# Optimization experiments

Measured on AMD Instinct MI355X. Metric: run time of the kernel, lower is better.

Reference implementation:

```python
import jax, jax.numpy as jnp
import numpy as np

D = 128          # voxel grid resolution per axis
N = 500_000      # number of active voxels
C = 64           # channels (in == out)
K = 27           # 3x3x3 kernel volume
EPS = 1e-5


def _build_geometry():
    """Random active voxel set + submanifold 3x3x3 neighbor index pairs."""
    rng = np.random.default_rng(0)
    lin = rng.choice(D ** 3, size=N, replace=False).astype(np.int64)
    zc, yc, xc = lin // (D * D), (lin // D) % D, lin % D
    order = np.argsort(lin)
    sorted_lin = lin[order]
    nbr = np.zeros((K, N), np.int32)
    valid = np.zeros((K, N), np.float32)
    k = 0
    for dz in (-1, 0, 1):
        for dy in (-1, 0, 1):
            for dx in (-1, 0, 1):
                nz, ny, nx = zc + dz, yc + dy, xc + dx
                inb = (nz >= 0) & (nz < D) & (ny >= 0) & (ny < D) & (nx >= 0) & (nx < D)
                nlin = nz * D * D + ny * D + nx
                pos = np.clip(np.searchsorted(sorted_lin, nlin), 0, N - 1)
                found = inb & (sorted_lin[pos] == nlin)
                nbr[k] = np.where(found, order[pos], 0).astype(np.int32)
                valid[k] = found.astype(np.float32)
                k += 1
    return jnp.asarray(nbr), jnp.asarray(valid)


def setup_inputs() -> dict:
    key = jax.random.key(0)
    k_feat, k_w1, k_w2 = jax.random.split(key, 3)
    nbr_idx, valid = _build_geometry()
    scale = 1.0 / np.sqrt(K * C)  # kaiming-ish fan-in init
    return {
        "features": jax.random.normal(k_feat, (N, C), jnp.float32),
        "nbr_idx": nbr_idx,
        "valid": valid,
        "W1": jax.random.normal(k_w1, (K, C, C), jnp.float32) * scale,
        "gamma1": jnp.ones((C,), jnp.float32),
        "beta1": jnp.zeros((C,), jnp.float32),
        "W2": jax.random.normal(k_w2, (K, C, C), jnp.float32) * scale,
        "gamma2": jnp.ones((C,), jnp.float32),
        "beta2": jnp.zeros((C,), jnp.float32),
    }


def _subm_conv(x, W, nbr_idx, valid):
    """Submanifold 3D conv as gather-GEMM-accumulate over K kernel offsets."""
    def step(acc, kw):
        Wk, nk, vk = kw
        return acc + (x[nk] * vk[:, None]) @ Wk, None  # [N,Cin] @ [Cin,Cout]
    acc0 = jnp.zeros((x.shape[0], W.shape[-1]), x.dtype)
    acc, _ = jax.lax.scan(step, acc0, (W, nbr_idx, valid))
    return acc


def _batchnorm(f, gamma, beta):
    """Training-mode BN over active voxels (biased variance, like torch)."""
    mean = jnp.mean(f, axis=0)
    var = jnp.mean(jnp.square(f - mean), axis=0)
    return (f - mean) * jax.lax.rsqrt(var + EPS) * gamma + beta


def reference(features, nbr_idx, valid, W1, gamma1, beta1, W2, gamma2, beta2):
    out = _subm_conv(features, W1, nbr_idx, valid)
    out = jax.nn.relu(_batchnorm(out, gamma1, beta1))
    out = _subm_conv(out, W2, nbr_idx, valid)
    out = _batchnorm(out, gamma2, beta2)
    return jax.nn.relu(out + features)  # identity shortcut (Cin==Cout, stride=1)
```

## Files before the change

### kernel.cpp

```cpp
#include <hip/hip_runtime.h>
#include <hip/hip_bf16.h>
#include <stdint.h>

typedef __attribute__((ext_vector_type(8))) short short8;
typedef __attribute__((ext_vector_type(4))) float floatx4;

__device__ __forceinline__ float bf2f(unsigned short u) {
    union { unsigned int ui; float f; } v; v.ui = ((unsigned int)u) << 16; return v.f;
}
__device__ __forceinline__ unsigned short f2bf(float f) {
    union { float f; unsigned int u; } v; v.f = f;
    unsigned int u = v.u;
    unsigned int r = (u + 0x7fffu + ((u >> 16) & 1u)) >> 16;
    return (unsigned short)r;
}

__global__ __launch_bounds__(256)
void convert_bf16(const float* __restrict__ in, unsigned short* __restrict__ out, int n4) {
    int i = blockIdx.x * blockDim.x + threadIdx.x;
    int stride = gridDim.x * blockDim.x;
    for (; i < n4; i += stride) {
        float4 v = ((const float4*)in)[i];
        ushort4 o;
        o.x = f2bf(v.x); o.y = f2bf(v.y); o.z = f2bf(v.z); o.w = f2bf(v.w);
        ((ushort4*)out)[i] = o;
    }
}

__global__ __launch_bounds__(256)
void encode_kernel(const int* __restrict__ nbr, const float* __restrict__ valid,
                   int* __restrict__ enc, int nvox, int nvoxp) {
    int k = blockIdx.y;
    int r = blockIdx.x * 256 + threadIdx.x;
    int v = -1;
    if (r < nvox) {
        float f = valid[(size_t)k * nvox + r];
        int ix = nbr[(size_t)k * nvox + r];
        v = (f != 0.f) ? ix : -1;
    }
    enc[(size_t)k * nvoxp + r] = v;
}

__global__ __launch_bounds__(256)
void pack_w(const float* __restrict__ W1, const float* __restrict__ W2,
            unsigned short* __restrict__ Wp1, unsigned short* __restrict__ Wp2) {
    int bi = blockIdx.x;
    const float* W = (bi < 27) ? W1 : W2;
    unsigned short* Wp = (bi < 27) ? Wp1 : Wp2;
    int kk = bi % 27;
    int t = threadIdx.x;
    int lane = t & 63, grp = t >> 6;
    int q = lane >> 4, l15 = lane & 15;
    for (int c8 = grp; c8 < 8; c8 += 4) {
        int ks = c8 >> 2, nt = c8 & 3;
        unsigned short* dst = Wp + (((kk*2 + ks)*4 + nt)*64 + lane)*8;
        const float* src = W + kk*4096 + (ks*32 + q*8)*64 + nt*16 + l15;
        #pragma unroll
        for (int j = 0; j < 8; ++j) dst[j] = f2bf(src[j*64]);
    }
}

__global__ __launch_bounds__(256, 4)
void conv_kernel(const unsigned short* __restrict__ xin, const int* __restrict__ enc,
                 const unsigned short* __restrict__ Wp, const unsigned short* __restrict__ zrow,
                 unsigned short* __restrict__ yout, float* __restrict__ sums,
                 int nvox, int nvoxp) {
    int t = threadIdx.x;
    int wave = t >> 6, lane = t & 63;
    int q = lane >> 4, l15 = lane & 15;
    int m0 = blockIdx.x * 256 + wave * 64;

    floatx4 acc[4][4];
    #pragma unroll
    for (int s = 0; s < 4; ++s)
        #pragma unroll
        for (int nt = 0; nt < 4; ++nt) acc[s][nt] = (floatx4){0.f, 0.f, 0.f, 0.f};

    for (int kk = 0; kk < 27; ++kk) {
        int e_all = enc[(size_t)kk * nvoxp + m0 + lane];
        const unsigned short* rp[4];
        #pragma unroll
        for (int s = 0; s < 4; ++s) {
            int es = __builtin_amdgcn_ds_bpermute((s*16 + l15) * 4, e_all);
            rp[s] = (es >= 0) ? (xin + (size_t)es * 64) : zrow;
        }
        short8 av[2][4];
        #pragma unroll
        for (int ks = 0; ks < 2; ++ks)
            #pragma unroll
            for (int s = 0; s < 4; ++s)
                av[ks][s] = *(const short8*)(rp[s] + ks*32 + q*8);

        #pragma unroll
        for (int ks = 0; ks < 2; ++ks) {
            const unsigned short* wb = Wp + ((kk*2 + ks)*4)*512 + lane*8;
            #pragma unroll
            for (int nt = 0; nt < 4; ++nt) {
                short8 bv = *(const short8*)(wb + nt*512);
                #pragma unroll
                for (int s = 0; s < 4; ++s)
                    acc[s][nt] = __builtin_amdgcn_mfma_f32_16x16x32_bf16(av[ks][s], bv, acc[s][nt], 0, 0, 0);
            }
        }
    }

    #pragma unroll
    for (int s = 0; s < 4; ++s) {
        int rowb = m0 + s*16 + q*4;
        #pragma unroll
        for (int r = 0; r < 4; ++r) {
            if (rowb + r < nvox) {
                unsigned short* yo = yout + (size_t)(rowb + r)*64 + l15;
                #pragma unroll
                for (int nt = 0; nt < 4; ++nt)
                    yo[nt*16] = f2bf(acc[s][nt][r]);
            }
        }
    }

    __shared__ float sred[128];
    if (t < 128) sred[t] = 0.f;
    __syncthreads();
    #pragma unroll
    for (int nt = 0; nt < 4; ++nt) {
        float s_ = 0.f, q_ = 0.f;
        #pragma unroll
        for (int s = 0; s < 4; ++s)
            #pragma unroll
            for (int r = 0; r < 4; ++r) {
                float v = acc[s][nt][r];
                s_ += v; q_ += v*v;
            }
        atomicAdd(&sred[nt*16 + l15], s_);
        atomicAdd(&sred[64 + nt*16 + l15], q_);
    }
    __syncthreads();
    if (t < 128) atomicAdd(&sums[t], sred[t]);
}

__global__ void finalize_kernel(const float* __restrict__ sums, const float* __restrict__ gamma,
                                const float* __restrict__ beta, float* __restrict__ ab, float invn) {
    int c = threadIdx.x;
    if (c < 64) {
        float mean = sums[c] * invn;
        float var  = sums[64 + c] * invn - mean*mean;
        float a = gamma[c] * rsqrtf(var + 1e-5f);
        ab[c] = a;
        ab[64 + c] = beta[c] - mean * a;
    }
}

__global__ __launch_bounds__(256)
void bnrelu_kernel(unsigned short* __restrict__ y, const float* __restrict__ ab, int n4) {
    int i = blockIdx.x * blockDim.x + threadIdx.x;
    int stride = gridDim.x * blockDim.x;
    for (; i < n4; i += stride) {
        uint2 v = ((const uint2*)y)[i];
        int c0 = (i*4) & 63;
        float f0 = fmaxf(ab[c0]   * bf2f((unsigned short)(v.x & 0xffffu)) + ab[64 + c0],   0.f);
        float f1 = fmaxf(ab[c0+1] * bf2f((unsigned short)(v.x >> 16))     + ab[64 + c0+1], 0.f);
        float f2 = fmaxf(ab[c0+2] * bf2f((unsigned short)(v.y & 0xffffu)) + ab[64 + c0+2], 0.f);
        float f3 = fmaxf(ab[c0+3] * bf2f((unsigned short)(v.y >> 16))     + ab[64 + c0+3], 0.f);
        uint2 o;
        o.x = (unsigned int)f2bf(f0) | ((unsigned int)f2bf(f1) << 16);
        o.y = (unsigned int)f2bf(f2) | ((unsigned int)f2bf(f3) << 16);
        ((uint2*)y)[i] = o;
    }
}

__global__ __launch_bounds__(256)
void final_kernel(const unsigned short* __restrict__ y2, const float* __restrict__ feat,
                  const float* __restrict__ ab, float* __restrict__ out, int ntot2) {
    int i = blockIdx.x * blockDim.x + threadIdx.x;
    int stride = gridDim.x * blockDim.x;
    for (; i < ntot2; i += stride) {
        unsigned int v = ((const unsigned int*)y2)[i];
        int c0 = (i*2) & 63;
        float2 f = ((const float2*)feat)[i];
        float r0 = fmaxf(ab[c0]   * bf2f((unsigned short)(v & 0xffffu)) + ab[64 + c0]   + f.x, 0.f);
        float r1 = fmaxf(ab[c0+1] * bf2f((unsigned short)(v >> 16))     + ab[64 + c0+1] + f.y, 0.f);
        ((float2*)out)[i] = make_float2(r0, r1);
    }
}

extern "C" void kernel_launch(void* const* d_in, const int* in_sizes, int n_in,
                              void* d_out, int out_size, void* d_ws, size_t ws_size,
                              hipStream_t stream) {
    const float* features = (const float*)d_in[0];
    const int*   nbr      = (const int*)d_in[1];
    const float* valid    = (const float*)d_in[2];
    const float* W1       = (const float*)d_in[3];
    const float* gamma1   = (const float*)d_in[4];
    const float* beta1    = (const float*)d_in[5];
    const float* W2       = (const float*)d_in[6];
    const float* gamma2   = (const float*)d_in[7];
    const float* beta2    = (const float*)d_in[8];
    float* out = (float*)d_out;

    int nvox  = in_sizes[0] / 64;
    int nvoxp = (nvox + 255) & ~255;
    size_t featB = (size_t)nvox * 64 * 2;

    char* ob = (char*)d_out;
    unsigned short* xb = (unsigned short*)ob;
    unsigned short* y1 = (unsigned short*)(ob + featB);

    char* ws = (char*)d_ws;
    float* stats = (float*)ws;
    float* sums1 = stats;
    float* sums2 = stats + 128;
    float* ab1   = stats + 256;
    float* ab2   = stats + 384;
    const unsigned short* zrow = (const unsigned short*)(ws + 2048);
    unsigned short* Wp1 = (unsigned short*)(ws + 4096);
    unsigned short* Wp2 = (unsigned short*)(ws + 4096 + 221184);
    int* enc = (int*)(ws + 524288);
    size_t encB = (size_t)27 * nvoxp * 4;
    unsigned short* y2 = (unsigned short*)(ws + 524288 + encB);

    hipMemsetAsync(ws, 0, 4096, stream);

    convert_bf16<<<2048, 256, 0, stream>>>(features, xb, nvox * 16);
    pack_w<<<54, 256, 0, stream>>>(W1, W2, Wp1, Wp2);
    dim3 eg(nvoxp / 256, 27);
    encode_kernel<<<eg, 256, 0, stream>>>(nbr, valid, enc, nvox, nvoxp);

    int convGrid = nvoxp / 256;
    conv_kernel<<<convGrid, 256, 0, stream>>>(xb, enc, Wp1, zrow, y1, sums1, nvox, nvoxp);
    finalize_kernel<<<1, 64, 0, stream>>>(sums1, gamma1, beta1, ab1, 1.0f / nvox);
    bnrelu_kernel<<<2048, 256, 0, stream>>>(y1, ab1, nvox * 16);
    conv_kernel<<<convGrid, 256, 0, stream>>>(y1, enc, Wp2, zrow, y2, sums2, nvox, nvoxp);
    finalize_kernel<<<1, 64, 0, stream>>>(sums2, gamma2, beta2, ab2, 1.0f / nvox);
    final_kernel<<<4096, 256, 0, stream>>>(y2, features, ab2, out, nvox * 32);
}
```

Measured before the change: 782.1 us.

## Double-buffer neighbor gathers against MFMA and stage neighbor indices in LDS

Each block now preloads all 27 neighbor-index rows for its 256 voxels into shared memory. The kernel-offset loop becomes a two-stage software pipeline: the gathered feature rows for the next offset are loaded into a second register buffer while MFMAs run on the current one, with sched barriers and raised wave priority around the MFMA phase. The aim is to hide the latency of random global gathers behind matrix math and to drop the per-iteration bpermute. In exchange it uses about 27 KB of LDS per block and twice the A-fragment registers, so the occupancy hint drops from 4 to 3 blocks.

```diff
diff --git a/kernel.cpp b/kernel.cpp
--- a/kernel.cpp
+++ b/kernel.cpp
@@ -60,49 +60,86 @@
     }
 }
 
-__global__ __launch_bounds__(256, 4)
+__global__ __launch_bounds__(256, 3)
 void conv_kernel(const unsigned short* __restrict__ xin, const int* __restrict__ enc,
                  const unsigned short* __restrict__ Wp, const unsigned short* __restrict__ zrow,
                  unsigned short* __restrict__ yout, float* __restrict__ sums,
                  int nvox, int nvoxp) {
+    __shared__ int lds_enc[27 * 256];
+    __shared__ float sred[128];
+
     int t = threadIdx.x;
     int wave = t >> 6, lane = t & 63;
     int q = lane >> 4, l15 = lane & 15;
     int m0 = blockIdx.x * 256 + wave * 64;
 
+    {
+        size_t base = (size_t)blockIdx.x * 256;
+        #pragma unroll
+        for (int kk = 0; kk < 27; ++kk)
+            lds_enc[kk * 256 + t] = enc[(size_t)kk * nvoxp + base + t];
+    }
+    if (t < 128) sred[t] = 0.f;
+    __syncthreads();
+
     floatx4 acc[4][4];
     #pragma unroll
     for (int s = 0; s < 4; ++s)
         #pragma unroll
         for (int nt = 0; nt < 4; ++nt) acc[s][nt] = (floatx4){0.f, 0.f, 0.f, 0.f};
 
-    for (int kk = 0; kk < 27; ++kk) {
-        int e_all = enc[(size_t)kk * nvoxp + m0 + lane];
-        const unsigned short* rp[4];
-        #pragma unroll
-        for (int s = 0; s < 4; ++s) {
-            int es = __builtin_amdgcn_ds_bpermute((s*16 + l15) * 4, e_all);
-            rp[s] = (es >= 0) ? (xin + (size_t)es * 64) : zrow;
-        }
-        short8 av[2][4];
-        #pragma unroll
-        for (int ks = 0; ks < 2; ++ks)
-            #pragma unroll
-            for (int s = 0; s < 4; ++s)
-                av[ks][s] = *(const short8*)(rp[s] + ks*32 + q*8);
-
-        #pragma unroll
-        for (int ks = 0; ks < 2; ++ks) {
-            const unsigned short* wb = Wp + ((kk*2 + ks)*4)*512 + lane*8;
-            #pragma unroll
-            for (int nt = 0; nt < 4; ++nt) {
-                short8 bv = *(const short8*)(wb + nt*512);
-                #pragma unroll
-                for (int s = 0; s < 4; ++s)
-                    acc[s][nt] = __builtin_amdgcn_mfma_f32_16x16x32_bf16(av[ks][s], bv, acc[s][nt], 0, 0, 0);
-            }
-        }
-    }
+    int eb = wave * 64 + l15;
+
+#define LOAD_ES(es, kk) { _Pragma("unroll") \
+    for (int s_ = 0; s_ < 4; ++s_) es[s_] = lds_enc[(kk) * 256 + eb + s_ * 16]; }
+
+#define GATHER(av, es) { _Pragma("unroll") \
+    for (int s_ = 0; s_ < 4; ++s_) { \
+        const unsigned short* rp_ = (es[s_] >= 0) ? (xin + (size_t)es[s_] * 64) : zrow; \
+        av[0][s_] = *(const short8*)(rp_ + q * 8); \
+        av[1][s_] = *(const short8*)(rp_ + 32 + q * 8); \
+    } }
+
+#define MFMA_PHASE(av, kk) { \
+    __builtin_amdgcn_s_setprio(1); \
+    _Pragma("unroll") for (int ks_ = 0; ks_ < 2; ++ks_) { \
+        const unsigned short* wb_ = Wp + (((kk) * 2 + ks_) * 4) * 512 + lane * 8; \
+        _Pragma("unroll") for (int nt_ = 0; nt_ < 4; ++nt_) { \
+            short8 bv_ = *(const short8*)(wb_ + nt_ * 512); \
+            _Pragma("unroll") for (int s_ = 0; s_ < 4; ++s_) \
+                acc[s_][nt_] = __builtin_amdgcn_mfma_f32_16x16x32_bf16(av[ks_][s_], bv_, acc[s_][nt_], 0, 0, 0); \
+        } \
+    } \
+    __builtin_amdgcn_s_setprio(0); \
+}
+
+    short8 avA[2][4], avB[2][4];
+    int esE[4], esO[4];
+
+    LOAD_ES(esE, 0);
+    LOAD_ES(esO, 1);
+    GATHER(avA, esE);
+    LOAD_ES(esE, 2);
+
+    #pragma unroll 1
+    for (int kkp = 0; kkp < 26; kkp += 2) {
+        GATHER(avB, esO);
+        int k3 = kkp + 3; if (k3 > 26) k3 = 26;
+        LOAD_ES(esO, k3);
+        __builtin_amdgcn_sched_barrier(0);
+        MFMA_PHASE(avA, kkp);
+
+        GATHER(avA, esE);
+        int k4 = kkp + 4; if (k4 > 26) k4 = 26;
+        LOAD_ES(esE, k4);
+        __builtin_amdgcn_sched_barrier(0);
+        MFMA_PHASE(avB, kkp + 1);
+    }
+    MFMA_PHASE(avA, 26);
+
+#undef LOAD_ES
+#undef GATHER
+#undef MFMA_PHASE
 
     #pragma unroll
     for (int s = 0; s < 4; ++s) {
@@ -118,9 +155,6 @@
         }
     }
 
-    __shared__ float sred[128];
-    if (t < 128) sred[t] = 0.f;
-    __syncthreads();
     #pragma unroll
     for (int nt = 0; nt < 4; ++nt) {
         float s_ = 0.f, q_ = 0.f;
```

Result: slower. 858.4 us (+9.8%).

## Software-pipeline gather loads in conv kernel with triple-buffered A fragments

Applied to the files above, without the earlier changes.

Restructures the conv kernel so each wave handles 32 rows instead of 64, doubling the grid. The gathers and enc index loads for later kernel offsets are issued two offsets ahead through three rotating register buffers, with sched_barrier and setprio around the MFMA phase. The aim is to hide gather latency behind MFMAs and raise the number of waves in flight. In exchange, each wave reloads the B weights for only 32 rows, so weight traffic per row doubles, and register pressure rises.

```diff
diff --git a/kernel.cpp b/kernel.cpp
--- a/kernel.cpp
+++ b/kernel.cpp
@@ -65,47 +65,83 @@
                  const unsigned short* __restrict__ Wp, const unsigned short* __restrict__ zrow,
                  unsigned short* __restrict__ yout, float* __restrict__ sums,
                  int nvox, int nvoxp) {
+    __shared__ float sred[128];
     int t = threadIdx.x;
     int wave = t >> 6, lane = t & 63;
     int q = lane >> 4, l15 = lane & 15;
-    int m0 = blockIdx.x * 256 + wave * 64;
-
-    floatx4 acc[4][4];
+    int m0 = blockIdx.x * 128 + wave * 32;
+    int qb = q * 8;
+
+    if (t < 128) sred[t] = 0.f;
+    __syncthreads();
+
+    floatx4 acc[2][4];
     #pragma unroll
-    for (int s = 0; s < 4; ++s)
+    for (int s = 0; s < 2; ++s)
         #pragma unroll
         for (int nt = 0; nt < 4; ++nt) acc[s][nt] = (floatx4){0.f, 0.f, 0.f, 0.f};
 
-    for (int kk = 0; kk < 27; ++kk) {
-        int e_all = enc[(size_t)kk * nvoxp + m0 + lane];
-        const unsigned short* rp[4];
-        #pragma unroll
-        for (int s = 0; s < 4; ++s) {
-            int es = __builtin_amdgcn_ds_bpermute((s*16 + l15) * 4, e_all);
-            rp[s] = (es >= 0) ? (xin + (size_t)es * 64) : zrow;
-        }
-        short8 av[2][4];
-        #pragma unroll
-        for (int ks = 0; ks < 2; ++ks)
-            #pragma unroll
-            for (int s = 0; s < 4; ++s)
-                av[ks][s] = *(const short8*)(rp[s] + ks*32 + q*8);
-
-        #pragma unroll
-        for (int ks = 0; ks < 2; ++ks) {
-            const unsigned short* wb = Wp + ((kk*2 + ks)*4)*512 + lane*8;
-            #pragma unroll
-            for (int nt = 0; nt < 4; ++nt) {
-                short8 bv = *(const short8*)(wb + nt*512);
-                #pragma unroll
-                for (int s = 0; s < 4; ++s)
-                    acc[s][nt] = __builtin_amdgcn_mfma_f32_16x16x32_bf16(av[ks][s], bv, acc[s][nt], 0, 0, 0);
-            }
-        }
-    }
+    short8 av0[2][2], av1[2][2], av2[2][2];
+    short8 bv[2][4];
+    int es0[2], es1[2], es2[2];
+
+#define ESLOAD(esX, kkv) { int kc_ = (kkv) > 26 ? 26 : (kkv); \
+    const int* ep_ = enc + (size_t)kc_ * nvoxp + m0 + l15; \
+    esX[0] = ep_[0]; esX[1] = ep_[16]; }
+
+#define GATHER(avX, esX) { _Pragma("unroll") for (int s_ = 0; s_ < 2; ++s_) { \
+    const unsigned short* rp_ = (esX[s_] >= 0) ? (xin + (size_t)esX[s_] * 64) : zrow; \
+    avX[0][s_] = *(const short8*)(rp_ + qb); \
+    avX[1][s_] = *(const short8*)(rp_ + 32 + qb); } }
+
+#define BLOAD(kkv) { const unsigned short* wq_ = Wp + (kkv) * 4096 + lane * 8; \
+    _Pragma("unroll") for (int ks_ = 0; ks_ < 2; ++ks_) \
+    _Pragma("unroll") for (int nt_ = 0; nt_ < 4; ++nt_) \
+        bv[ks_][nt_] = *(const short8*)(wq_ + ks_ * 2048 + nt_ * 512); }
+
+#define MFMA_PHASE(avX) { __builtin_amdgcn_s_setprio(1); \
+    _Pragma("unroll") for (int ks_ = 0; ks_ < 2; ++ks_) \
+    _Pragma("unroll") for (int nt_ = 0; nt_ < 4; ++nt_) { \
+        acc[0][nt_] = __builtin_amdgcn_mfma_f32_16x16x32_bf16(avX[ks_][0], bv[ks_][nt_], acc[0][nt_], 0, 0, 0); \
+        acc[1][nt_] = __builtin_amdgcn_mfma_f32_16x16x32_bf16(avX[ks_][1], bv[ks_][nt_], acc[1][nt_], 0, 0, 0); } \
+    __builtin_amdgcn_s_setprio(0); }
+
+    ESLOAD(es0, 0); ESLOAD(es1, 1); ESLOAD(es2, 2);
+    GATHER(av0, es0);
+    ESLOAD(es0, 3);
+    GATHER(av1, es1);
+    ESLOAD(es1, 4);
+
+    #pragma unroll 1
+    for (int it = 0; it < 9; ++it) {
+        int kk = it * 3;
+
+        BLOAD(kk);
+        GATHER(av2, es2);
+        ESLOAD(es2, kk + 5);
+        __builtin_amdgcn_sched_barrier(0);
+        MFMA_PHASE(av0);
+
+        BLOAD(kk + 1);
+        GATHER(av0, es0);
+        ESLOAD(es0, kk + 6);
+        __builtin_amdgcn_sched_barrier(0);
+        MFMA_PHASE(av1);
+
+        BLOAD(kk + 2);
+        GATHER(av1, es1);
+        ESLOAD(es1, kk + 7);
+        __builtin_amdgcn_sched_barrier(0);
+        MFMA_PHASE(av2);
+    }
+
+#undef ESLOAD
+#undef GATHER
+#undef BLOAD
+#undef MFMA_PHASE
 
     #pragma unroll
-    for (int s = 0; s < 4; ++s) {
+    for (int s = 0; s < 2; ++s) {
         int rowb = m0 + s*16 + q*4;
         #pragma unroll
         for (int r = 0; r < 4; ++r) {
@@ -118,14 +154,11 @@
         }
     }
 
-    __shared__ float sred[128];
-    if (t < 128) sred[t] = 0.f;
-    __syncthreads();
     #pragma unroll
     for (int nt = 0; nt < 4; ++nt) {
         float s_ = 0.f, q_ = 0.f;
         #pragma unroll
-        for (int s = 0; s < 4; ++s)
+        for (int s = 0; s < 2; ++s)
             #pragma unroll
             for (int r = 0; r < 4; ++r) {
                 float v = acc[s][nt][r];
@@ -225,7 +258,7 @@
     dim3 eg(nvoxp / 256, 27);
     encode_kernel<<<eg, 256, 0, stream>>>(nbr, valid, enc, nvox, nvoxp);
 
-    int convGrid = nvoxp / 256;
+    int convGrid = nvoxp / 128;
     conv_kernel<<<convGrid, 256, 0, stream>>>(xb, enc, Wp1, zrow, y1, sums1, nvox, nvoxp);
     finalize_kernel<<<1, 64, 0, stream>>>(sums1, gamma1, beta1, ab1, 1.0f / nvox);
     bnrelu_kernel<<<2048, 256, 0, stream>>>(y1, ab1, nvox * 16);
```

After: 1.271 ms. +62.5%, slower.
